# Performance work log

Hardware: AMD Instinct MI355X
Metric: run time of the kernel (lower is better)

Reference implementation:

```python
import jax, jax.numpy as jnp
import numpy as np

ALPHA = 50.0  # softmax temperature from __init__
EPS = 1e-12   # torch F.normalize eps


def _l2norm(v, axis):
    return v / jnp.maximum(jnp.linalg.norm(v, axis=axis, keepdims=True), EPS)


def setup_inputs() -> dict:
    key = jax.random.key(0)
    k1, k2 = jax.random.split(key)
    N, C, H, W, K = 64, 512, 32, 32, 64
    x = jax.random.normal(k1, (N, C, H, W), jnp.float32)
    # conv.weight after _init_params has shape (dim, num_clusters) = (C, K)
    conv_weight = jax.random.normal(k2, (C, K), jnp.float32) * 0.05
    conv_bias = jnp.zeros((K,), jnp.float32)
    return {"x": x, "conv_weight": conv_weight, "conv_bias": conv_bias}


def reference(x, conv_weight, conv_bias):
    N, C, H, W = x.shape
    HW = H * W
    # normalize_input=True: L2 normalize over channel dim
    xn = _l2norm(x, axis=1)
    xf = xn.reshape(N, C, HW)                      # [N, C, HW]
    # column-normalized projection weight (F.normalize(conv.weight, dim=0))
    Wn = _l2norm(conv_weight, axis=0)              # [C, K]
    # soft assignment logits: x^T Wn -> stored as [N, K, HW]
    sa_logits = jnp.einsum('nch,ck->nkh', xf, Wn)  # [N, K, HW]
    soft_assign = jax.nn.softmax((sa_logits + conv_bias[None, :, None]) * ALPHA, axis=1)
    # VLAD via two batched contractions instead of the [N,K,C,HW] residual tensor:
    # sum_h a[n,k,h] * (x[n,:,h] - W[:,k]) = (a @ x^T)[n,k,:] - (sum_h a) * W[:,k]
    vlad = jnp.einsum('nkh,nch->nkc', soft_assign, xf) \
         - soft_assign.sum(-1)[..., None] * conv_weight.T[None]   # [N, K, C]
    vlad = _l2norm(vlad, axis=2).reshape(N, -1)    # intra-norm + flatten -> [N, K*C]
    feature = jnp.transpose(xf, (0, 2, 1))         # [N, HW, C]
    return (vlad, sa_logits, feature)
```

## Files before the change

kernel.cpp:

```cpp
#include <hip/hip_runtime.h>
#include <math.h>

#define N_   64
#define C_   512
#define HW_  1024
#define K_   64
#define ALPHA_ 50.0f
#define EPS_  1e-12f

#define OUT_VLAD 0
#define OUT_SA   2097152
#define OUT_FEAT 6291456

#define WSB_WT    0
#define WSB_WNTB  131072
#define WSB_INVN  196608
#define WSB_A     458752
#define WSB_SAP   8847360
#define WSB_PART  9109504
#define PART_ELEMS 2097152

typedef __attribute__((ext_vector_type(8))) __bf16 bf16x8;
typedef __attribute__((ext_vector_type(4))) float f32x4;
typedef __attribute__((ext_vector_type(8))) unsigned short ushort8v;

__device__ inline unsigned short f2bf(float f) {
    unsigned int u = __builtin_bit_cast(unsigned int, f);
    u = (u + 0x7FFFu + ((u >> 16) & 1u)) >> 16;
    return (unsigned short)u;
}
__device__ inline float bf2f(unsigned short h) {
    unsigned int u = ((unsigned int)h) << 16;
    return __builtin_bit_cast(float, u);
}
__device__ inline f32x4 mfma16(const unsigned short* pa, const unsigned short* pb, f32x4 c) {
    bf16x8 a = *(const bf16x8*)pa;
    bf16x8 b = *(const bf16x8*)pb;
    return __builtin_amdgcn_mfma_f32_16x16x32_bf16(a, b, c, 0, 0, 0);
}

__global__ __launch_bounds__(256) void k1_weights(const float* __restrict__ W,
                                                  float* __restrict__ wT,
                                                  unsigned short* __restrict__ wnTb) {
    int k = blockIdx.x;
    int t = threadIdx.x;
    __shared__ float red[256];
    float s = 0.f;
    for (int c = t; c < C_; c += 256) { float w = W[c * K_ + k]; s += w * w; }
    red[t] = s;
    __syncthreads();
    for (int st = 128; st > 0; st >>= 1) {
        if (t < st) red[t] += red[t + st];
        __syncthreads();
    }
    float inv = 1.f / fmaxf(sqrtf(red[0]), EPS_);
    for (int c = t; c < C_; c += 256) {
        float w = W[c * K_ + k];
        wT[k * C_ + c]   = w;
        wnTb[k * C_ + c] = f2bf(w * inv);
    }
}

__global__ __launch_bounds__(256) void k2_normfeat(const float* __restrict__ x,
                                                   float* __restrict__ out,
                                                   float* __restrict__ invn) {
    float* feat = out + OUT_FEAT;
    int b   = blockIdx.x;
    int n   = b >> 6;
    int hw0 = (b & 63) << 4;
    int t   = threadIdx.x;
    __shared__ float Xs[C_ * 17 + 256 + 16];
    float* red = Xs + C_ * 17;
    float* nrm = red + 256;
    const float* xn = x + (long)n * C_ * HW_;
    for (int j = 0; j < 32; ++j) {
        int idx = j * 256 + t;
        int c = idx >> 4, p = idx & 15;
        Xs[c * 17 + p] = xn[c * HW_ + hw0 + p];
    }
    __syncthreads();
    {
        int p = t & 15, cg = t >> 4;
        float s = 0.f;
        for (int j = 0; j < 32; ++j) {
            float v = Xs[(cg + 16 * j) * 17 + p];
            s += v * v;
        }
        red[t] = s;
    }
    __syncthreads();
    if (t < 16) {
        float s = 0.f;
        for (int g = 0; g < 16; ++g) s += red[g * 16 + t];
        float iv = 1.f / fmaxf(sqrtf(s), EPS_);
        nrm[t] = iv;
        invn[(long)n * HW_ + hw0 + t] = iv;
    }
    __syncthreads();
    float* frow = feat + ((long)n * HW_ + hw0) * C_;
    for (int p = 0; p < 16; ++p) {
        float iv = nrm[p];
        frow[(long)p * C_ + t]       = Xs[t * 17 + p] * iv;
        frow[(long)p * C_ + t + 256] = Xs[(t + 256) * 17 + p] * iv;
    }
}

#define K3PITCH 136
__global__ __launch_bounds__(256, 4) void k3_sa(const float* __restrict__ feat,
                                                const unsigned short* __restrict__ wnTb,
                                                const float* __restrict__ bias,
                                                float* __restrict__ sa,
                                                unsigned short* __restrict__ Ab,
                                                float* __restrict__ sumA_part) {
    __shared__ alignas(16) unsigned short sm[64 * K3PITCH + 64 * K3PITCH];
    unsigned short* Fsh = sm;
    unsigned short* Wsh = sm + 64 * K3PITCH;
    float* Ls = (float*)sm;
    float* Bz = Ls + 64 * 66;
    float* Zm = Bz + 64;
    float* Iv = Zm + 64;
    float* Rm = Iv + 64;
    float* Rs = Rm + 256;

    int b    = blockIdx.x;
    int n    = b >> 4;
    int tile = b & 15;
    int hw0  = tile << 6;
    int t    = threadIdx.x;
    int l    = t & 63, w = t >> 6;
    int mr   = l & 15, q = l >> 4;

    f32x4 acc[4];
#pragma unroll
    for (int j = 0; j < 4; ++j) acc[j] = (f32x4){0.f, 0.f, 0.f, 0.f};

    const float* fb = feat + ((long)n * HW_ + hw0) * C_;
    for (int ch = 0; ch < 4; ++ch) {
        int c0 = ch * 128;
        __syncthreads();
#pragma unroll
        for (int j = 0; j < 4; ++j) {
            int idx = j * 256 + t;
            int row = idx >> 4, sg = idx & 15;
            const float* src = fb + (long)row * C_ + c0 + sg * 8;
            float4 v0 = *(const float4*)src;
            float4 v1 = *(const float4*)(src + 4);
            ushort8v pk;
            pk[0] = f2bf(v0.x); pk[1] = f2bf(v0.y); pk[2] = f2bf(v0.z); pk[3] = f2bf(v0.w);
            pk[4] = f2bf(v1.x); pk[5] = f2bf(v1.y); pk[6] = f2bf(v1.z); pk[7] = f2bf(v1.w);
            *(ushort8v*)(Fsh + row * K3PITCH + sg * 8) = pk;
        }
#pragma unroll
        for (int j = 0; j < 4; ++j) {
            int idx = j * 256 + t;
            int row = idx >> 4, sg = idx & 15;
            *(uint4*)(Wsh + row * K3PITCH + sg * 8) =
                *(const uint4*)(wnTb + row * C_ + c0 + sg * 8);
        }
        __syncthreads();
#pragma unroll
        for (int ks = 0; ks < 4; ++ks) {
            int ko = ks * 32 + q * 8;
            const unsigned short* ap = Fsh + (w * 16 + mr) * K3PITCH + ko;
#pragma unroll
            for (int j = 0; j < 4; ++j) {
                const unsigned short* bp = Wsh + (j * 16 + mr) * K3PITCH + ko;
                acc[j] = mfma16(ap, bp, acc[j]);
            }
        }
    }
    __syncthreads();
#pragma unroll
    for (int j = 0; j < 4; ++j)
#pragma unroll
        for (int r = 0; r < 4; ++r)
            Ls[(j * 16 + mr) * 66 + w * 16 + q * 4 + r] = acc[j][r];
    if (t < 64) Bz[t] = bias[t];
    __syncthreads();
    {
        int p = t & 63, g = t >> 6;
        float mx = -1e30f;
#pragma unroll
        for (int kk = 0; kk < 16; ++kk) {
            int kc = g * 16 + kk;
            float z = (Ls[kc * 66 + p] + Bz[kc]) * ALPHA_;
            mx = fmaxf(mx, z);
        }
        Rm[g * 64 + p] = mx;
        __syncthreads();
        float M = fmaxf(fmaxf(Rm[p], Rm[64 + p]), fmaxf(Rm[128 + p], Rm[192 + p]));
        float s = 0.f;
#pragma unroll
        for (int kk = 0; kk < 16; ++kk) {
            int kc = g * 16 + kk;
            float z = (Ls[kc * 66 + p] + Bz[kc]) * ALPHA_;
            s += __expf(z - M);
        }
        Rs[g * 64 + p] = s;
        __syncthreads();
        if (g == 0) {
            Zm[p] = M;
            Iv[p] = 1.f / (Rs[p] + Rs[64 + p] + Rs[128 + p] + Rs[192 + p]);
        }
    }
    __syncthreads();
    float* sab = sa + (long)n * K_ * HW_ + hw0;
    unsigned short* Arow = Ab + (long)n * K_ * HW_ + hw0;
#pragma unroll
    for (int j = 0; j < 16; ++j) {
        int idx = j * 256 + t;
        int kc = idx >> 6, p = idx & 63;
        float v = Ls[kc * 66 + p];
        sab[(long)kc * HW_ + p] = v;
        float a = __expf((v + Bz[kc]) * ALPHA_ - Zm[p]) * Iv[p];
        Arow[(long)kc * HW_ + p] = f2bf(a);
        Ls[kc * 66 + p] = a;
    }
    __syncthreads();
    if (t < 64) {
        float s = 0.f;
        for (int p2 = 0; p2 < 64; ++p2) s += Ls[t * 66 + p2];
        sumA_part[((long)n * 16 + tile) * 64 + t] = s;
    }
}

#define K4PITCH 72
__global__ __launch_bounds__(256, 4) void k4_vlad(const float* __restrict__ x,
                                                  const float* __restrict__ invn,
                                                  const unsigned short* __restrict__ Ab,
                                                  float* __restrict__ part) {
    __shared__ float invs[512];
    __shared__ alignas(16) unsigned short Ash[64 * K4PITCH];
    __shared__ alignas(16) unsigned short Fsh[64 * K4PITCH];
    int b  = blockIdx.x;
    int n  = b >> 4;
    int r  = b & 15;
    int c_off  = (r & 7) * 64;
    int hh     = r >> 3;
    int h_base = hh * 512;
    int t = threadIdx.x;
    int l = t & 63, w = t >> 6;
    int mr = l & 15, q = l >> 4;
    int kcb = (w >> 1) * 32, cb = (w & 1) * 32;

    invs[t]       = invn[(long)n * HW_ + h_base + t];
    invs[t + 256] = invn[(long)n * HW_ + h_base + 256 + t];

    f32x4 acc[2][2];
#pragma unroll
    for (int i = 0; i < 2; ++i)
#pragma unroll
        for (int j = 0; j < 2; ++j) acc[i][j] = (f32x4){0.f, 0.f, 0.f, 0.f};

    const unsigned short* Abase = Ab + (long)n * K_ * HW_ + h_base;
    const float* xbase = x + ((long)n * C_ + c_off) * HW_ + h_base;

    for (int ch = 0; ch < 8; ++ch) {
        int h0 = ch * 64;
        __syncthreads();
#pragma unroll
        for (int j = 0; j < 2; ++j) {
            int idx = j * 256 + t;
            int row = idx >> 3, sg = idx & 7;
            *(uint4*)(Ash + row * K4PITCH + sg * 8) =
                *(const uint4*)(Abase + (long)row * HW_ + h0 + sg * 8);
        }
#pragma unroll
        for (int j = 0; j < 2; ++j) {
            int idx = j * 256 + t;
            int row = idx >> 3, sg = idx & 7;
            const float* src = xbase + (long)row * HW_ + h0 + sg * 8;
            float4 v0 = *(const float4*)src;
            float4 v1 = *(const float4*)(src + 4);
            const float* iv = invs + h0 + sg * 8;
            ushort8v pk;
            pk[0] = f2bf(v0.x * iv[0]); pk[1] = f2bf(v0.y * iv[1]);
            pk[2] = f2bf(v0.z * iv[2]); pk[3] = f2bf(v0.w * iv[3]);
            pk[4] = f2bf(v1.x * iv[4]); pk[5] = f2bf(v1.y * iv[5]);
            pk[6] = f2bf(v1.z * iv[6]); pk[7] = f2bf(v1.w * iv[7]);
            *(ushort8v*)(Fsh + row * K4PITCH + sg * 8) = pk;
        }
        __syncthreads();
#pragma unroll
        for (int ks = 0; ks < 2; ++ks) {
            int ko = ks * 32 + q * 8;
            const unsigned short* ap0 = Ash + (kcb + mr) * K4PITCH + ko;
            const unsigned short* ap1 = Ash + (kcb + 16 + mr) * K4PITCH + ko;
#pragma unroll
            for (int j = 0; j < 2; ++j) {
                const unsigned short* bp = Fsh + (cb + j * 16 + mr) * K4PITCH + ko;
                acc[0][j] = mfma16(ap0, bp, acc[0][j]);
                acc[1][j] = mfma16(ap1, bp, acc[1][j]);
            }
        }
    }
    float* pb = part + (long)hh * PART_ELEMS + (long)n * K_ * C_ + c_off;
#pragma unroll
    for (int i = 0; i < 2; ++i)
#pragma unroll
        for (int j = 0; j < 2; ++j)
#pragma unroll
            for (int rr = 0; rr < 4; ++rr) {
                int kc = kcb + i * 16 + q * 4 + rr;
                int c  = cb + j * 16 + mr;
                pb[(long)kc * C_ + c] = acc[i][j][rr];
            }
}

__global__ __launch_bounds__(256) void k5_norm(const float* __restrict__ part,
                                               const float* __restrict__ sumA_part,
                                               const float* __restrict__ wT,
                                               float* __restrict__ vlad) {
    __shared__ float red[256];
    __shared__ float sred[16];
    int row = blockIdx.x;
    int kc  = row & 63;
    int n   = row >> 6;
    int t   = threadIdx.x;
    if (t < 16) sred[t] = sumA_part[((long)n * 16 + t) * 64 + kc];
    __syncthreads();
    float sA = 0.f;
#pragma unroll
    for (int i = 0; i < 16; ++i) sA += sred[i];
    long base = (long)row * C_;
    float v0, v1;
    {
        int c = t;
        float s = part[base + c] + part[PART_ELEMS + base + c];
        v0 = s - sA * wT[kc * C_ + c];
    }
    {
        int c = t + 256;
        float s = part[base + c] + part[PART_ELEMS + base + c];
        v1 = s - sA * wT[kc * C_ + c];
    }
    red[t] = v0 * v0 + v1 * v1;
    __syncthreads();
    for (int st = 128; st > 0; st >>= 1) {
        if (t < st) red[t] += red[t + st];
        __syncthreads();
    }
    float inv = 1.f / fmaxf(sqrtf(red[0]), EPS_);
    vlad[base + t]       = v0 * inv;
    vlad[base + t + 256] = v1 * inv;
}

extern "C" void kernel_launch(void* const* d_in, const int* in_sizes, int n_in,
                              void* d_out, int out_size, void* d_ws, size_t ws_size,
                              hipStream_t stream) {
    const float* x    = (const float*)d_in[0];
    const float* W    = (const float*)d_in[1];
    const float* bias = (const float*)d_in[2];
    float* out = (float*)d_out;
    char* wsb  = (char*)d_ws;

    float* wT            = (float*)(wsb + WSB_WT);
    unsigned short* wnTb = (unsigned short*)(wsb + WSB_WNTB);
    float* invn          = (float*)(wsb + WSB_INVN);
    unsigned short* Ab   = (unsigned short*)(wsb + WSB_A);
    float* sumA_part     = (float*)(wsb + WSB_SAP);
    float* part          = (float*)(wsb + WSB_PART);

    float* vlad = out + OUT_VLAD;
    float* sa   = out + OUT_SA;
    float* feat = out + OUT_FEAT;

    hipLaunchKernelGGL(k1_weights,  dim3(64),   dim3(256), 0, stream, W, wT, wnTb);
    hipLaunchKernelGGL(k2_normfeat, dim3(4096), dim3(256), 0, stream, x, out, invn);
    hipLaunchKernelGGL(k3_sa,       dim3(1024), dim3(256), 0, stream, feat, wnTb, bias, sa, Ab, sumA_part);
    hipLaunchKernelGGL(k4_vlad,     dim3(1024), dim3(256), 0, stream, x, invn, Ab, part);
    hipLaunchKernelGGL(k5_norm,     dim3(4096), dim3(256), 0, stream, part, sumA_part, wT, vlad);
}
```

Measured before the change: 344.5 us.

## Precompute bf16 normalized features in both layouts for downstream GEMMs

The normalization kernel now also writes bf16 copies of the normalized features, in [HW,C] and [C,HW] layouts. The soft-assignment and VLAD kernels then load bf16 directly instead of reading fp32 and converting, and the inverse-norm buffer is removed. The soft-assign epilogue also vectorizes its stores to two elements per thread. This trades extra writes in k2 for halved reads and less conversion work in k3/k4.

```diff
diff --git a/kernel.cpp b/kernel.cpp
--- a/kernel.cpp
+++ b/kernel.cpp
@@ -14,24 +14,20 @@
 
 #define WSB_WT    0
 #define WSB_WNTB  131072
-#define WSB_INVN  196608
-#define WSB_A     458752
-#define WSB_SAP   8847360
-#define WSB_PART  9109504
+#define WSB_A     196608
+#define WSB_SAP   8585216
+#define WSB_PART  8847360
+#define WSB_FEATB 25624576
+#define WSB_XNB   92733440
 #define PART_ELEMS 2097152
 
 typedef __attribute__((ext_vector_type(8))) __bf16 bf16x8;
 typedef __attribute__((ext_vector_type(4))) float f32x4;
-typedef __attribute__((ext_vector_type(8))) unsigned short ushort8v;
 
 __device__ inline unsigned short f2bf(float f) {
     unsigned int u = __builtin_bit_cast(unsigned int, f);
     u = (u + 0x7FFFu + ((u >> 16) & 1u)) >> 16;
     return (unsigned short)u;
-}
-__device__ inline float bf2f(unsigned short h) {
-    unsigned int u = ((unsigned int)h) << 16;
-    return __builtin_bit_cast(float, u);
 }
 __device__ inline f32x4 mfma16(const unsigned short* pa, const unsigned short* pb, f32x4 c) {
     bf16x8 a = *(const bf16x8*)pa;
@@ -63,7 +59,8 @@
 
 __global__ __launch_bounds__(256) void k2_normfeat(const float* __restrict__ x,
                                                    float* __restrict__ out,
-                                                   float* __restrict__ invn) {
+                                                   unsigned short* __restrict__ featb,
+                                                   unsigned short* __restrict__ xnb) {
     float* feat = out + OUT_FEAT;
     int b   = blockIdx.x;
     int n   = b >> 6;
@@ -92,9 +89,7 @@
     if (t < 16) {
         float s = 0.f;
         for (int g = 0; g < 16; ++g) s += red[g * 16 + t];
-        float iv = 1.f / fmaxf(sqrtf(s), EPS_);
-        nrm[t] = iv;
-        invn[(long)n * HW_ + hw0 + t] = iv;
+        nrm[t] = 1.f / fmaxf(sqrtf(s), EPS_);
     }
     __syncthreads();
     float* frow = feat + ((long)n * HW_ + hw0) * C_;
@@ -103,10 +98,27 @@
         frow[(long)p * C_ + t]       = Xs[t * 17 + p] * iv;
         frow[(long)p * C_ + t + 256] = Xs[(t + 256) * 17 + p] * iv;
     }
+    unsigned int* fbp = (unsigned int*)featb;
+    for (int j = 0; j < 16; ++j) {
+        int idx = j * 256 + t;
+        int p = idx >> 8, cp = idx & 255;
+        float iv = nrm[p];
+        unsigned int lo = f2bf(Xs[(2 * cp) * 17 + p] * iv);
+        unsigned int hi = f2bf(Xs[(2 * cp + 1) * 17 + p] * iv);
+        fbp[((long)n * HW_ + hw0 + p) * 256 + cp] = lo | (hi << 16);
+    }
+    unsigned int* xbp = (unsigned int*)xnb;
+    for (int j = 0; j < 16; ++j) {
+        int idx = j * 256 + t;
+        int c = idx >> 3, hp = idx & 7;
+        unsigned int lo = f2bf(Xs[c * 17 + 2 * hp]     * nrm[2 * hp]);
+        unsigned int hi = f2bf(Xs[c * 17 + 2 * hp + 1] * nrm[2 * hp + 1]);
+        xbp[((long)n * C_ + c) * 512 + (hw0 >> 1) + hp] = lo | (hi << 16);
+    }
 }
 
 #define K3PITCH 136
-__global__ __launch_bounds__(256, 4) void k3_sa(const float* __restrict__ feat,
+__global__ __launch_bounds__(256, 4) void k3_sa(const unsigned short* __restrict__ featb,
                                                 const unsigned short* __restrict__ wnTb,
                                                 const float* __restrict__ bias,
                                                 float* __restrict__ sa,
@@ -134,7 +146,7 @@
 #pragma unroll
     for (int j = 0; j < 4; ++j) acc[j] = (f32x4){0.f, 0.f, 0.f, 0.f};
 
-    const float* fb = feat + ((long)n * HW_ + hw0) * C_;
+    const unsigned short* fb = featb + ((long)n * HW_ + hw0) * C_;
     for (int ch = 0; ch < 4; ++ch) {
         int c0 = ch * 128;
         __syncthreads();
@@ -142,13 +154,8 @@
         for (int j = 0; j < 4; ++j) {
             int idx = j * 256 + t;
             int row = idx >> 4, sg = idx & 15;
-            const float* src = fb + (long)row * C_ + c0 + sg * 8;
-            float4 v0 = *(const float4*)src;
-            float4 v1 = *(const float4*)(src + 4);
-            ushort8v pk;
-            pk[0] = f2bf(v0.x); pk[1] = f2bf(v0.y); pk[2] = f2bf(v0.z); pk[3] = f2bf(v0.w);
-            pk[4] = f2bf(v1.x); pk[5] = f2bf(v1.y); pk[6] = f2bf(v1.z); pk[7] = f2bf(v1.w);
-            *(ushort8v*)(Fsh + row * K3PITCH + sg * 8) = pk;
+            *(uint4*)(Fsh + row * K3PITCH + sg * 8) =
+                *(const uint4*)(fb + (long)row * C_ + c0 + sg * 8);
         }
 #pragma unroll
         for (int j = 0; j < 4; ++j) {
@@ -207,14 +214,18 @@
     float* sab = sa + (long)n * K_ * HW_ + hw0;
     unsigned short* Arow = Ab + (long)n * K_ * HW_ + hw0;
 #pragma unroll
-    for (int j = 0; j < 16; ++j) {
+    for (int j = 0; j < 8; ++j) {
         int idx = j * 256 + t;
-        int kc = idx >> 6, p = idx & 63;
-        float v = Ls[kc * 66 + p];
-        sab[(long)kc * HW_ + p] = v;
-        float a = __expf((v + Bz[kc]) * ALPHA_ - Zm[p]) * Iv[p];
-        Arow[(long)kc * HW_ + p] = f2bf(a);
-        Ls[kc * 66 + p] = a;
+        int kc = idx >> 5, pp = idx & 31;
+        int p = pp * 2;
+        float2 v = *(const float2*)(Ls + kc * 66 + p);
+        *(float2*)(sab + (long)kc * HW_ + p) = v;
+        float a0 = __expf((v.x + Bz[kc]) * ALPHA_ - Zm[p])     * Iv[p];
+        float a1 = __expf((v.y + Bz[kc]) * ALPHA_ - Zm[p + 1]) * Iv[p + 1];
+        *(unsigned int*)(Arow + (long)kc * HW_ + p) =
+            (unsigned int)f2bf(a0) | ((unsigned int)f2bf(a1) << 16);
+        Ls[kc * 66 + p]     = a0;
+        Ls[kc * 66 + p + 1] = a1;
     }
     __syncthreads();
     if (t < 64) {
@@ -225,11 +236,9 @@
 }
 
 #define K4PITCH 72
-__global__ __launch_bounds__(256, 4) void k4_vlad(const float* __restrict__ x,
-                                                  const float* __restrict__ invn,
+__global__ __launch_bounds__(256, 4) void k4_vlad(const unsigned short* __restrict__ xnb,
                                                   const unsigned short* __restrict__ Ab,
                                                   float* __restrict__ part) {
-    __shared__ float invs[512];
     __shared__ alignas(16) unsigned short Ash[64 * K4PITCH];
     __shared__ alignas(16) unsigned short Fsh[64 * K4PITCH];
     int b  = blockIdx.x;
@@ -243,9 +252,6 @@
     int mr = l & 15, q = l >> 4;
     int kcb = (w >> 1) * 32, cb = (w & 1) * 32;
 
-    invs[t]       = invn[(long)n * HW_ + h_base + t];
-    invs[t + 256] = invn[(long)n * HW_ + h_base + 256 + t];
-
     f32x4 acc[2][2];
 #pragma unroll
     for (int i = 0; i < 2; ++i)
@@ -253,7 +259,7 @@
         for (int j = 0; j < 2; ++j) acc[i][j] = (f32x4){0.f, 0.f, 0.f, 0.f};
 
     const unsigned short* Abase = Ab + (long)n * K_ * HW_ + h_base;
-    const float* xbase = x + ((long)n * C_ + c_off) * HW_ + h_base;
+    const unsigned short* xb    = xnb + ((long)n * C_ + c_off) * HW_ + h_base;
 
     for (int ch = 0; ch < 8; ++ch) {
         int h0 = ch * 64;
@@ -269,16 +275,8 @@
         for (int j = 0; j < 2; ++j) {
             int idx = j * 256 + t;
             int row = idx >> 3, sg = idx & 7;
-            const float* src = xbase + (long)row * HW_ + h0 + sg * 8;
-            float4 v0 = *(const float4*)src;
-            float4 v1 = *(const float4*)(src + 4);
-            const float* iv = invs + h0 + sg * 8;
-            ushort8v pk;
-            pk[0] = f2bf(v0.x * iv[0]); pk[1] = f2bf(v0.y * iv[1]);
-            pk[2] = f2bf(v0.z * iv[2]); pk[3] = f2bf(v0.w * iv[3]);
-            pk[4] = f2bf(v1.x * iv[4]); pk[5] = f2bf(v1.y * iv[5]);
-            pk[6] = f2bf(v1.z * iv[6]); pk[7] = f2bf(v1.w * iv[7]);
-            *(ushort8v*)(Fsh + row * K4PITCH + sg * 8) = pk;
+            *(uint4*)(Fsh + row * K4PITCH + sg * 8) =
+                *(const uint4*)(xb + (long)row * HW_ + h0 + sg * 8);
         }
         __syncthreads();
 #pragma unroll
@@ -356,18 +354,18 @@
 
     float* wT            = (float*)(wsb + WSB_WT);
     unsigned short* wnTb = (unsigned short*)(wsb + WSB_WNTB);
-    float* invn          = (float*)(wsb + WSB_INVN);
     unsigned short* Ab   = (unsigned short*)(wsb + WSB_A);
     float* sumA_part     = (float*)(wsb + WSB_SAP);
     float* part          = (float*)(wsb + WSB_PART);
+    unsigned short* featb = (unsigned short*)(wsb + WSB_FEATB);
+    unsigned short* xnb   = (unsigned short*)(wsb + WSB_XNB);
 
     float* vlad = out + OUT_VLAD;
     float* sa   = out + OUT_SA;
-    float* feat = out + OUT_FEAT;
 
     hipLaunchKernelGGL(k1_weights,  dim3(64),   dim3(256), 0, stream, W, wT, wnTb);
-    hipLaunchKernelGGL(k2_normfeat, dim3(4096), dim3(256), 0, stream, x, out, invn);
-    hipLaunchKernelGGL(k3_sa,       dim3(1024), dim3(256), 0, stream, feat, wnTb, bias, sa, Ab, sumA_part);
-    hipLaunchKernelGGL(k4_vlad,     dim3(1024), dim3(256), 0, stream, x, invn, Ab, part);
+    hipLaunchKernelGGL(k2_normfeat, dim3(4096), dim3(256), 0, stream, x, out, featb, xnb);
+    hipLaunchKernelGGL(k3_sa,       dim3(1024), dim3(256), 0, stream, featb, wnTb, bias, sa, Ab, sumA_part);
+    hipLaunchKernelGGL(k4_vlad,     dim3(1024), dim3(256), 0, stream, xnb, Ab, part);
     hipLaunchKernelGGL(k5_norm,     dim3(4096), dim3(256), 0, stream, part, sumA_part, wT, vlad);
 }
```

After: 378.2 us. +9.8%, slower.

## Fuse channel normalization and soft-assignment GEMM into one kernel

Applied to the files above, without the earlier changes.

Merges the normalize/transposed-feature kernel with the soft-assignment MFMA kernel. The normalized tile stays in shared memory as bf16, so the feature tensor is no longer re-read from global memory. Each block now covers 16 spatial positions instead of 64, so the weight tile is reloaded four times as often and sumA partials grow to 64 per batch, with k5 reducing more partials. Occupancy drops to 3 blocks per CU and only one wave's MFMA results are used, leaving other waves idle during the GEMM.

```diff
diff --git a/kernel.cpp b/kernel.cpp
--- a/kernel.cpp
+++ b/kernel.cpp
@@ -17,7 +17,7 @@
 #define WSB_INVN  196608
 #define WSB_A     458752
 #define WSB_SAP   8847360
-#define WSB_PART  9109504
+#define WSB_PART  9895936
 #define PART_ELEMS 2097152
 
 typedef __attribute__((ext_vector_type(8))) __bf16 bf16x8;
@@ -28,10 +28,6 @@
     unsigned int u = __builtin_bit_cast(unsigned int, f);
     u = (u + 0x7FFFu + ((u >> 16) & 1u)) >> 16;
     return (unsigned short)u;
-}
-__device__ inline float bf2f(unsigned short h) {
-    unsigned int u = ((unsigned int)h) << 16;
-    return __builtin_bit_cast(float, u);
 }
 __device__ inline f32x4 mfma16(const unsigned short* pa, const unsigned short* pb, f32x4 c) {
     bf16x8 a = *(const bf16x8*)pa;
@@ -61,80 +57,87 @@
     }
 }
 
-__global__ __launch_bounds__(256) void k2_normfeat(const float* __restrict__ x,
-                                                   float* __restrict__ out,
-                                                   float* __restrict__ invn) {
-    float* feat = out + OUT_FEAT;
-    int b   = blockIdx.x;
-    int n   = b >> 6;
-    int hw0 = (b & 63) << 4;
-    int t   = threadIdx.x;
-    __shared__ float Xs[C_ * 17 + 256 + 16];
-    float* red = Xs + C_ * 17;
-    float* nrm = red + 256;
-    const float* xn = x + (long)n * C_ * HW_;
-    for (int j = 0; j < 32; ++j) {
-        int idx = j * 256 + t;
-        int c = idx >> 4, p = idx & 15;
-        Xs[c * 17 + p] = xn[c * HW_ + hw0 + p];
-    }
-    __syncthreads();
-    {
+#define FPITCH 520
+#define LSP    20
+__global__ __launch_bounds__(256, 3) void k23_fused(const float* __restrict__ x,
+                                                    const unsigned short* __restrict__ wnTb,
+                                                    const float* __restrict__ bias,
+                                                    float* __restrict__ out,
+                                                    float* __restrict__ invn,
+                                                    unsigned short* __restrict__ Ab,
+                                                    float* __restrict__ sumA_part) {
+    __shared__ alignas(16) char smraw[32768 + 128 + 16640];
+    float* Xs            = (float*)smraw;
+    unsigned short* Wsh  = (unsigned short*)smraw;
+    float* invsh         = (float*)(smraw + 32768);
+    unsigned short* FshB = (unsigned short*)(smraw + 32896);
+    f32x4* red4          = (f32x4*)(smraw + 32896);
+    float* Ls            = (float*)(smraw + 32896);
+    float* Bz = Ls + 64 * LSP;
+    float* Zm = Bz + 64;
+    float* Iv = Zm + 16;
+    float* Rm = Iv + 16;
+    float* Rs = Rm + 288;
+
+    int b = blockIdx.x;
+    int n = b >> 6, tile = b & 63;
+    int hw0 = tile << 4;
+    int t = threadIdx.x;
+    int l = t & 63;
+    int mr = l & 15, q = l >> 4;
+
+    const float* xb = x + (long)n * C_ * HW_ + hw0;
+    int qv = t & 3, cbase = t >> 2;
+    int qs = qv ^ (cbase & 3);
+    f32x4 sq = (f32x4){0.f, 0.f, 0.f, 0.f};
+    f32x4* Xs4 = (f32x4*)Xs;
+#pragma unroll
+    for (int j = 0; j < 8; ++j) {
+        int c = cbase + 64 * j;
+        f32x4 v = *(const f32x4*)(xb + (long)c * HW_ + qv * 4);
+        sq += v * v;
+        Xs4[c * 4 + qs] = v;
+    }
+    red4[t] = sq;
+    __syncthreads();
+    if (t < 128) red4[t] += red4[t + 128]; __syncthreads();
+    if (t < 64)  red4[t] += red4[t + 64];  __syncthreads();
+    if (t < 32)  red4[t] += red4[t + 32];  __syncthreads();
+    if (t < 16)  red4[t] += red4[t + 16];  __syncthreads();
+    if (t < 8)   red4[t] += red4[t + 8];   __syncthreads();
+    if (t < 4)   red4[t] += red4[t + 4];   __syncthreads();
+    if (t < 16) {
+        float s  = ((float*)red4)[t];
+        float iv = 1.f / fmaxf(sqrtf(s), EPS_);
+        invsh[t] = iv;
+        invn[(long)n * HW_ + hw0 + t] = iv;
+    }
+    __syncthreads();
+
+    {
+        float* frow = out + OUT_FEAT + ((long)n * HW_ + hw0) * C_;
         int p = t & 15, cg = t >> 4;
-        float s = 0.f;
-        for (int j = 0; j < 32; ++j) {
-            float v = Xs[(cg + 16 * j) * 17 + p];
-            s += v * v;
-        }
-        red[t] = s;
-    }
-    __syncthreads();
-    if (t < 16) {
-        float s = 0.f;
-        for (int g = 0; g < 16; ++g) s += red[g * 16 + t];
-        float iv = 1.f / fmaxf(sqrtf(s), EPS_);
-        nrm[t] = iv;
-        invn[(long)n * HW_ + hw0 + t] = iv;
-    }
-    __syncthreads();
-    float* frow = feat + ((long)n * HW_ + hw0) * C_;
-    for (int p = 0; p < 16; ++p) {
-        float iv = nrm[p];
-        frow[(long)p * C_ + t]       = Xs[t * 17 + p] * iv;
-        frow[(long)p * C_ + t + 256] = Xs[(t + 256) * 17 + p] * iv;
-    }
-}
-
-#define K3PITCH 136
-__global__ __launch_bounds__(256, 4) void k3_sa(const float* __restrict__ feat,
-                                                const unsigned short* __restrict__ wnTb,
-                                                const float* __restrict__ bias,
-                                                float* __restrict__ sa,
-                                                unsigned short* __restrict__ Ab,
-                                                float* __restrict__ sumA_part) {
-    __shared__ alignas(16) unsigned short sm[64 * K3PITCH + 64 * K3PITCH];
-    unsigned short* Fsh = sm;
-    unsigned short* Wsh = sm + 64 * K3PITCH;
-    float* Ls = (float*)sm;
-    float* Bz = Ls + 64 * 66;
-    float* Zm = Bz + 64;
-    float* Iv = Zm + 64;
-    float* Rm = Iv + 64;
-    float* Rs = Rm + 256;
-
-    int b    = blockIdx.x;
-    int n    = b >> 4;
-    int tile = b & 15;
-    int hw0  = tile << 6;
-    int t    = threadIdx.x;
-    int l    = t & 63, w = t >> 6;
-    int mr   = l & 15, q = l >> 4;
+        float iv = invsh[p];
+        int ql = p >> 2, pr = p & 3;
+#pragma unroll
+        for (int j = 0; j < 8; ++j) {
+            int c0 = 64 * j + cg * 4;
+            float f0 = Xs[(c0    ) * 16 + ((ql ^ 0) << 2) + pr] * iv;
+            float f1 = Xs[(c0 + 1) * 16 + ((ql ^ 1) << 2) + pr] * iv;
+            float f2 = Xs[(c0 + 2) * 16 + ((ql ^ 2) << 2) + pr] * iv;
+            float f3 = Xs[(c0 + 3) * 16 + ((ql ^ 3) << 2) + pr] * iv;
+            f32x4 fv = (f32x4){f0, f1, f2, f3};
+            *(f32x4*)(frow + (long)p * C_ + c0) = fv;
+            uint2 u;
+            u.x = (unsigned)f2bf(f0) | ((unsigned)f2bf(f1) << 16);
+            u.y = (unsigned)f2bf(f2) | ((unsigned)f2bf(f3) << 16);
+            *(uint2*)(FshB + p * FPITCH + c0) = u;
+        }
+    }
 
     f32x4 acc[4];
 #pragma unroll
     for (int j = 0; j < 4; ++j) acc[j] = (f32x4){0.f, 0.f, 0.f, 0.f};
-
-    const float* fb = feat + ((long)n * HW_ + hw0) * C_;
     for (int ch = 0; ch < 4; ++ch) {
         int c0 = ch * 128;
         __syncthreads();
@@ -142,85 +145,95 @@
         for (int j = 0; j < 4; ++j) {
             int idx = j * 256 + t;
             int row = idx >> 4, sg = idx & 15;
-            const float* src = fb + (long)row * C_ + c0 + sg * 8;
-            float4 v0 = *(const float4*)src;
-            float4 v1 = *(const float4*)(src + 4);
-            ushort8v pk;
-            pk[0] = f2bf(v0.x); pk[1] = f2bf(v0.y); pk[2] = f2bf(v0.z); pk[3] = f2bf(v0.w);
-            pk[4] = f2bf(v1.x); pk[5] = f2bf(v1.y); pk[6] = f2bf(v1.z); pk[7] = f2bf(v1.w);
-            *(ushort8v*)(Fsh + row * K3PITCH + sg * 8) = pk;
-        }
-#pragma unroll
-        for (int j = 0; j < 4; ++j) {
-            int idx = j * 256 + t;
-            int row = idx >> 4, sg = idx & 15;
-            *(uint4*)(Wsh + row * K3PITCH + sg * 8) =
+            *(uint4*)(Wsh + row * 136 + sg * 8) =
                 *(const uint4*)(wnTb + row * C_ + c0 + sg * 8);
         }
         __syncthreads();
 #pragma unroll
         for (int ks = 0; ks < 4; ++ks) {
-            int ko = ks * 32 + q * 8;
-            const unsigned short* ap = Fsh + (w * 16 + mr) * K3PITCH + ko;
+            const unsigned short* ap = FshB + mr * FPITCH + c0 + ks * 32 + q * 8;
 #pragma unroll
             for (int j = 0; j < 4; ++j) {
-                const unsigned short* bp = Wsh + (j * 16 + mr) * K3PITCH + ko;
+                const unsigned short* bp = Wsh + (j * 16 + mr) * 136 + ks * 32 + q * 8;
                 acc[j] = mfma16(ap, bp, acc[j]);
             }
         }
     }
     __syncthreads();
+
 #pragma unroll
     for (int j = 0; j < 4; ++j)
 #pragma unroll
         for (int r = 0; r < 4; ++r)
-            Ls[(j * 16 + mr) * 66 + w * 16 + q * 4 + r] = acc[j][r];
+            Ls[(j * 16 + mr) * LSP + q * 4 + r] = acc[j][r];
     if (t < 64) Bz[t] = bias[t];
     __syncthreads();
     {
-        int p = t & 63, g = t >> 6;
+        int p = t & 15, g = t >> 4;
         float mx = -1e30f;
 #pragma unroll
-        for (int kk = 0; kk < 16; ++kk) {
-            int kc = g * 16 + kk;
-            float z = (Ls[kc * 66 + p] + Bz[kc]) * ALPHA_;
+        for (int kk = 0; kk < 4; ++kk) {
+            int kc = g * 4 + kk;
+            float z = (Ls[kc * LSP + p] + Bz[kc]) * ALPHA_;
             mx = fmaxf(mx, z);
         }
-        Rm[g * 64 + p] = mx;
-        __syncthreads();
-        float M = fmaxf(fmaxf(Rm[p], Rm[64 + p]), fmaxf(Rm[128 + p], Rm[192 + p]));
+        Rm[g * 18 + p] = mx;
+    }
+    __syncthreads();
+    if (t < 16) {
+        float M = -1e30f;
+#pragma unroll
+        for (int g = 0; g < 16; ++g) M = fmaxf(M, Rm[g * 18 + t]);
+        Zm[t] = M;
+    }
+    __syncthreads();
+    {
+        int p = t & 15, g = t >> 4;
+        float M = Zm[p];
         float s = 0.f;
 #pragma unroll
-        for (int kk = 0; kk < 16; ++kk) {
-            int kc = g * 16 + kk;
-            float z = (Ls[kc * 66 + p] + Bz[kc]) * ALPHA_;
+        for (int kk = 0; kk < 4; ++kk) {
+            int kc = g * 4 + kk;
+            float z = (Ls[kc * LSP + p] + Bz[kc]) * ALPHA_;
             s += __expf(z - M);
         }
-        Rs[g * 64 + p] = s;
-        __syncthreads();
-        if (g == 0) {
-            Zm[p] = M;
-            Iv[p] = 1.f / (Rs[p] + Rs[64 + p] + Rs[128 + p] + Rs[192 + p]);
-        }
-    }
-    __syncthreads();
-    float* sab = sa + (long)n * K_ * HW_ + hw0;
+        Rs[g * 18 + p] = s;
+    }
+    __syncthreads();
+    if (t < 16) {
+        float S = 0.f;
+#pragma unroll
+        for (int g = 0; g < 16; ++g) S += Rs[g * 18 + t];
+        Iv[t] = 1.f / S;
+    }
+    __syncthreads();
+
+    float* sab = out + OUT_SA + (long)n * K_ * HW_ + hw0;
     unsigned short* Arow = Ab + (long)n * K_ * HW_ + hw0;
-#pragma unroll
-    for (int j = 0; j < 16; ++j) {
-        int idx = j * 256 + t;
-        int kc = idx >> 6, p = idx & 63;
-        float v = Ls[kc * 66 + p];
-        sab[(long)kc * HW_ + p] = v;
-        float a = __expf((v + Bz[kc]) * ALPHA_ - Zm[p]) * Iv[p];
-        Arow[(long)kc * HW_ + p] = f2bf(a);
-        Ls[kc * 66 + p] = a;
+    {
+        int kc = t >> 2, p0 = (t & 3) * 4;
+        f32x4 v = *(f32x4*)(Ls + kc * LSP + p0);
+        *(f32x4*)(sab + (long)kc * HW_ + p0) = v;
+        float bz = Bz[kc];
+        float a0 = __expf((v[0] + bz) * ALPHA_ - Zm[p0])     * Iv[p0];
+        float a1 = __expf((v[1] + bz) * ALPHA_ - Zm[p0 + 1]) * Iv[p0 + 1];
+        float a2 = __expf((v[2] + bz) * ALPHA_ - Zm[p0 + 2]) * Iv[p0 + 2];
+        float a3 = __expf((v[3] + bz) * ALPHA_ - Zm[p0 + 3]) * Iv[p0 + 3];
+        uint2 u;
+        u.x = (unsigned)f2bf(a0) | ((unsigned)f2bf(a1) << 16);
+        u.y = (unsigned)f2bf(a2) | ((unsigned)f2bf(a3) << 16);
+        *(uint2*)(Arow + (long)kc * HW_ + p0) = u;
+        Ls[kc * LSP + p0]     = a0;
+        Ls[kc * LSP + p0 + 1] = a1;
+        Ls[kc * LSP + p0 + 2] = a2;
+        Ls[kc * LSP + p0 + 3] = a3;
     }
     __syncthreads();
     if (t < 64) {
         float s = 0.f;
-        for (int p2 = 0; p2 < 64; ++p2) s += Ls[t * 66 + p2];
-        sumA_part[((long)n * 16 + tile) * 64 + t] = s;
+#pragma unroll
+        for (int p = 0; p < 16; ++p) s += Ls[t * LSP + p];
+        sumA_part[((long)n * 64 + tile) * 64 + t] = s;
     }
 }
 
@@ -312,16 +325,18 @@
                                                const float* __restrict__ wT,
                                                float* __restrict__ vlad) {
     __shared__ float red[256];
-    __shared__ float sred[16];
+    __shared__ float sred[64];
     int row = blockIdx.x;
     int kc  = row & 63;
     int n   = row >> 6;
     int t   = threadIdx.x;
-    if (t < 16) sred[t] = sumA_part[((long)n * 16 + t) * 64 + kc];
-    __syncthreads();
-    float sA = 0.f;
-#pragma unroll
-    for (int i = 0; i < 16; ++i) sA += sred[i];
+    if (t < 64) sred[t] = sumA_part[((long)n * 64 + t) * 64 + kc];
+    __syncthreads();
+    if (t < 16) sred[t] = sred[t] + sred[t + 16] + sred[t + 32] + sred[t + 48];
+    __syncthreads();
+    if (t < 4) sred[t] = sred[t] + sred[t + 4] + sred[t + 8] + sred[t + 12];
+    __syncthreads();
+    float sA = sred[0] + sred[1] + sred[2] + sred[3];
     long base = (long)row * C_;
     float v0, v1;
     {
@@ -362,12 +377,9 @@
     float* part          = (float*)(wsb + WSB_PART);
 
     float* vlad = out + OUT_VLAD;
-    float* sa   = out + OUT_SA;
-    float* feat = out + OUT_FEAT;
-
-    hipLaunchKernelGGL(k1_weights,  dim3(64),   dim3(256), 0, stream, W, wT, wnTb);
-    hipLaunchKernelGGL(k2_normfeat, dim3(4096), dim3(256), 0, stream, x, out, invn);
-    hipLaunchKernelGGL(k3_sa,       dim3(1024), dim3(256), 0, stream, feat, wnTb, bias, sa, Ab, sumA_part);
-    hipLaunchKernelGGL(k4_vlad,     dim3(1024), dim3(256), 0, stream, x, invn, Ab, part);
-    hipLaunchKernelGGL(k5_norm,     dim3(4096), dim3(256), 0, stream, part, sumA_part, wT, vlad);
-}
+
+    hipLaunchKernelGGL(k1_weights, dim3(64),   dim3(256), 0, stream, W, wT, wnTb);
+    hipLaunchKernelGGL(k23_fused,  dim3(4096), dim3(256), 0, stream, x, wnTb, bias, out, invn, Ab, sumA_part);
+    hipLaunchKernelGGL(k4_vlad,    dim3(1024), dim3(256), 0, stream, x, invn, Ab, part);
+    hipLaunchKernelGGL(k5_norm,    dim3(4096), dim3(256), 0, stream, part, sumA_part, wT, vlad);
+}
```

Result: no change. 339.0 us (-1.6%).
